# Kernel optimization log

Hardware: AMD Instinct MI355X
Metric: run time of the kernel (lower is better)

Reference implementation:

```python
import jax, jax.numpy as jnp
import numpy as np

B, D, A = 512, 32, 10
NUM_CODES, CODE_DIM = 512, 64
COMMIT = 0.25


def _conv(x, w, b):
    # NHWC input, HWIO kernel, SAME padding, stride 1 (flax nn.Conv defaults)
    y = jax.lax.conv_general_dilated(x, w, (1, 1), 'SAME',
                                     dimension_numbers=('NHWC', 'HWIO', 'NHWC'))
    return y + b


def setup_inputs() -> dict:
    key = jax.random.key(0)
    ks = jax.random.split(key, 16)
    def rn(k, shape, scale):
        return jax.random.normal(k, shape, dtype=jnp.float32) * scale
    inp = {
        'x': rn(ks[0], (B, D, D), 1.0),
        'conv1_w': rn(ks[1], (3, 3, 1, 32), 0.3),
        'conv1_b': jnp.zeros((32,), jnp.float32),
        'conv2_w': rn(ks[2], (3, 3, 32, 64), 0.06),
        'conv2_b': jnp.zeros((64,), jnp.float32),
        'codebook': rn(ks[3], (NUM_CODES, CODE_DIM), 0.12),  # variance_scaling fan_in-ish
        'w1': rn(ks[4], (D * D * 64, 128), 0.004),
        'b1': jnp.zeros((128,), jnp.float32),
        'w2': rn(ks[5], (128, 128), 0.09),
        'b2': jnp.zeros((128,), jnp.float32),
        'w3': rn(ks[6], (128, 128), 0.09),
        'b3': jnp.zeros((128,), jnp.float32),
        'wa1': rn(ks[7], (128, 128), 0.09),
        'ba1': jnp.zeros((128,), jnp.float32),
        'wa2': rn(ks[8], (128, A), 0.09),
        'ba2': jnp.zeros((A,), jnp.float32),
        'wc1': rn(ks[9], (128, 128), 0.09),
        'bc1': jnp.zeros((128,), jnp.float32),
        'wc2': rn(ks[10], (128, 128), 0.09),
        'bc2': jnp.zeros((128,), jnp.float32),
        'wc3': rn(ks[11], (128, 1), 0.09),
        'bc3': jnp.zeros((1,), jnp.float32),
    }
    return inp


def reference(x, conv1_w, conv1_b, conv2_w, conv2_b, codebook,
              w1, b1, w2, b2, w3, b3,
              wa1, ba1, wa2, ba2,
              wc1, bc1, wc2, bc2, wc3, bc3):
    h = x.reshape(-1, D, D, 1)
    h = jax.nn.relu(_conv(h, conv1_w, conv1_b))
    h = jax.nn.relu(_conv(h, conv2_w, conv2_b))  # [B, D, D, 64]

    # --- Vector quantization (cdist + argmin + gather, straight-through) ---
    flat = h.reshape(-1, CODE_DIM)  # [B*D*D, 64]
    distances = (jnp.sum(flat ** 2, axis=1, keepdims=True)
                 - 2.0 * flat @ codebook.T
                 + jnp.sum(codebook ** 2, axis=1)[None, :])  # [N, num_codes]
    encoding_indices = jnp.argmin(distances, axis=1)
    quantized = codebook[encoding_indices].reshape(h.shape)
    quantized = h + jax.lax.stop_gradient(quantized - h)  # straight-through
    e_latent = jnp.mean((jax.lax.stop_gradient(quantized) - h) ** 2)
    q_latent = jnp.mean((quantized - jax.lax.stop_gradient(h)) ** 2)
    vq_loss = q_latent + COMMIT * e_latent

    # --- MLP trunk + actor-critic heads ---
    emb = quantized.reshape(quantized.shape[0], -1)
    emb = jax.nn.relu(emb @ w1 + b1)
    emb = jax.nn.relu(emb @ w2 + b2)
    emb = jax.nn.relu(emb @ w3 + b3)

    a = jax.nn.relu(emb @ wa1 + ba1)
    probs = jax.nn.softmax(a @ wa2 + ba2, axis=-1)  # Categorical probs

    c = jax.nn.relu(emb @ wc1 + bc1)
    c = jax.nn.relu(c @ wc2 + bc2)
    value = jnp.squeeze(c @ wc3 + bc3, axis=-1)

    return probs, value, vq_loss, encoding_indices
```

## Files before the change

kernel.cpp:

```cpp
#include <hip/hip_runtime.h>
#include <math.h>

#define NB 512
#define DD 32
#define NPX 1024
#define NTOT 524288
#define NC 512
#define CD 64

typedef float v2f __attribute__((ext_vector_type(2)));
typedef _Float16 hf;
typedef hf hf8 __attribute__((ext_vector_type(8)));
typedef float f32x4 __attribute__((ext_vector_type(4)));

__device__ __forceinline__ v2f pkfma(v2f a, v2f b, v2f c) {
    return __builtin_elementwise_fma(a, b, c);
}
__device__ __forceinline__ v2f splat2(float s) { v2f r; r.x = s; r.y = s; return r; }

__device__ __forceinline__ f32x4 mfma16(hf8 a, hf8 b, f32x4 c) {
    return __builtin_amdgcn_mfma_f32_16x16x32_f16(a, b, c, 0, 0, 0);
}

__device__ __forceinline__ float np_sumsq64(const float* a, int stride) {
    float r[8];
    #pragma unroll
    for (int j = 0; j < 8; ++j) {
        float v = a[j * stride];
        r[j] = __fmul_rn(v, v);
    }
    #pragma unroll
    for (int i = 1; i < 8; ++i)
        #pragma unroll
        for (int j = 0; j < 8; ++j) {
            float v = a[(i * 8 + j) * stride];
            r[j] = __fadd_rn(r[j], __fmul_rn(v, v));
        }
    return __fadd_rn(__fadd_rn(__fadd_rn(r[0], r[1]), __fadd_rn(r[2], r[3])),
                     __fadd_rn(__fadd_rn(r[4], r[5]), __fadd_rn(r[6], r[7])));
}

__global__ __launch_bounds__(256) void k_conv1(const float* __restrict__ x,
                                               const float* __restrict__ w,
                                               const float* __restrict__ bias,
                                               float* __restrict__ h1,
                                               const float* __restrict__ cb,
                                               const float* __restrict__ c2w,
                                               const float* __restrict__ w1,
                                               float* __restrict__ cnorm,
                                               hf* __restrict__ cbh,
                                               hf* __restrict__ cbl,
                                               hf* __restrict__ wTh,
                                               hf* __restrict__ wTl,
                                               hf* __restrict__ w1h,
                                               hf* __restrict__ w1l,
                                               float* __restrict__ accv) {
    const int b = blockIdx.x;
    const int tid = threadIdx.x;
    {
        int t = b * 256 + tid;
        if (t < NC)
            cnorm[t] = np_sumsq64(cb + (size_t)t * CD, 1);
        if (b < 128) {
            float a = cb[t] * 256.f;
            hf h0 = (hf)a;
            float rl = (a - (float)h0) * 2048.f;
            cbh[t] = h0;
            cbl[t] = (hf)rl;
        }
        if (b >= 128 && b < 200) {
            int t2 = (b - 128) * 256 + tid;
            if (t2 < 18432) {
                int s9 = t2 >> 11, rem = t2 & 2047;
                int co = rem >> 5, ci = rem & 31;
                float a = c2w[s9 * 2048 + ci * 64 + co] * 256.f;
                hf h0 = (hf)a;
                float rl = (a - (float)h0) * 2048.f;
                wTh[t2] = h0;
                wTl[t2] = (hf)rl;
            }
        }
        if (b >= 200 && b < 456) {
            int t3 = (b - 200) * 256 + tid;
            int n = t3 & 127;
            int k8b = (t3 >> 7) * 16;
            for (int kk = 0; kk < 16; ++kk) {
                int k8 = k8b + kk;
                hf vh[8], vl[8];
                #pragma unroll
                for (int j = 0; j < 8; ++j) {
                    float a = w1[(size_t)(k8 * 8 + j) * 128 + n] * 256.f;
                    hf h0 = (hf)a;
                    float rl = (a - (float)h0) * 2048.f;
                    vh[j] = h0;
                    vl[j] = (hf)rl;
                }
                *(hf8*)(w1h + (size_t)k8 * 1024 + n * 8) = *(hf8*)vh;
                *(hf8*)(w1l + (size_t)k8 * 1024 + n * 8) = *(hf8*)vl;
            }
        }
        if (t == 0) accv[0] = 0.f;
    }
    __shared__ float xs[34][34];
    for (int i = tid; i < 34 * 34; i += 256) {
        int yy = i / 34, xx = i - yy * 34;
        float v = 0.f;
        if (yy >= 1 && yy <= 32 && xx >= 1 && xx <= 32)
            v = x[(size_t)b * NPX + (yy - 1) * 32 + (xx - 1)];
        xs[yy][xx] = v;
    }
    __syncthreads();
    for (int rep = 0; rep < 4; ++rep) {
        int px = tid + rep * 256;
        int y = px >> 5, xc = px & 31;
        v2f acc2[16];
        #pragma unroll
        for (int c = 0; c < 16; ++c) acc2[c] = splat2(0.f);
        #pragma unroll
        for (int dy = 0; dy < 3; ++dy)
        #pragma unroll
        for (int dx = 0; dx < 3; ++dx) {
            float a = xs[y + dy][xc + dx];
            v2f av = splat2(a);
            const v2f* wr = (const v2f*)(w + (dy * 3 + dx) * 32);
            #pragma unroll
            for (int c = 0; c < 16; ++c) acc2[c] = pkfma(av, wr[c], acc2[c]);
        }
        float4* out = (float4*)(h1 + ((size_t)b * NPX + px) * 32);
        #pragma unroll
        for (int q = 0; q < 8; ++q) {
            float4 v;
            v.x = fmaxf(__fadd_rn(acc2[q*2+0].x, bias[q*4+0]), 0.f);
            v.y = fmaxf(__fadd_rn(acc2[q*2+0].y, bias[q*4+1]), 0.f);
            v.z = fmaxf(__fadd_rn(acc2[q*2+1].x, bias[q*4+2]), 0.f);
            v.w = fmaxf(__fadd_rn(acc2[q*2+1].y, bias[q*4+3]), 0.f);
            out[q] = v;
        }
    }
}

#define CI_P 40
#define TAU 2e-4f
__global__ __launch_bounds__(512, 2) void k_cvq(const float* __restrict__ h1,
                                                const hf* __restrict__ wTh,
                                                const hf* __restrict__ wTl,
                                                const float* __restrict__ c2w,
                                                const float* __restrict__ c2b,
                                                const float* __restrict__ cb,
                                                const hf* __restrict__ cbh,
                                                const hf* __restrict__ cbl,
                                                const float* __restrict__ cnorm,
                                                int* __restrict__ idxout,
                                                float* __restrict__ fidx,
                                                float* __restrict__ lossacc) {
    __shared__ hf Ah[10 * 34 * CI_P];
    __shared__ hf Al[10 * 34 * CI_P];
    __shared__ float4 Ats[16][256];
    __shared__ float cn_lds[512];
    __shared__ int   mis_lds[256];
    __shared__ int   rlist[256];
    __shared__ float hex[8][64];
    __shared__ int   rcnt;
    const int blk = blockIdx.x;
    const int b = blk >> 2, strip = blk & 3;
    const int r0 = strip * 8;
    const int tid = threadIdx.x;
    const size_t base = (size_t)blk * 256;
    if (tid == 0) rcnt = 0;
    cn_lds[tid] = cnorm[tid];
    for (int i = tid; i < 640; i += 512) {
        int ci = i & 31, rem = i >> 5;
        int ry = rem >> 1, colx = (rem & 1) * 33;
        int idx = (ry * 34 + colx) * CI_P + ci;
        Ah[idx] = (hf)0.f;
        Al[idx] = (hf)0.f;
    }
    #pragma unroll
    for (int r = 0; r < 5; ++r) {
        int j = tid + r * 512;
        int ci4 = j & 7, xc = (j >> 3) & 31, ry = j >> 8;
        int gy = r0 - 1 + ry;
        float4 v = make_float4(0.f, 0.f, 0.f, 0.f);
        if (gy >= 0 && gy < 32)
            v = *(const float4*)(h1 + ((size_t)b * NPX + gy * 32 + xc) * 32 + ci4 * 4);
        int bi = (ry * 34 + xc + 1) * CI_P + ci4 * 4;
        float fv[4] = {v.x, v.y, v.z, v.w};
        #pragma unroll
        for (int q = 0; q < 4; ++q) {
            float a = fv[q] * 256.f;
            hf h0 = (hf)a;
            float rl = (a - (float)h0) * 2048.f;
            Ah[bi + q] = h0;
            Al[bi + q] = (hf)rl;
        }
    }
    __syncthreads();
    const int w = tid >> 6, l = tid & 63;
    const int co16 = l & 15, g = l >> 4;
    #pragma unroll 1
    for (int ntp = 0; ntp < 2; ++ntp) {
        f32x4 hi[2][2], mid[2][2], llt[2][2];
        #pragma unroll
        for (int s = 0; s < 2; ++s)
            #pragma unroll
            for (int n = 0; n < 2; ++n) {
                hi[s][n] = f32x4{0.f, 0.f, 0.f, 0.f};
                mid[s][n] = f32x4{0.f, 0.f, 0.f, 0.f};
                llt[s][n] = f32x4{0.f, 0.f, 0.f, 0.f};
            }
        #pragma unroll 1
        for (int s9 = 0; s9 < 9; ++s9) {
            const int dy = s9 / 3, dx = s9 - dy * 3;
            hf8 a_h[2], a_l[2];
            #pragma unroll
            for (int s = 0; s < 2; ++s) {
                int ofs = ((w + dy) * 34 + (s * 16 + co16 + dx)) * CI_P + 8 * g;
                a_h[s] = *(const hf8*)(Ah + ofs);
                a_l[s] = *(const hf8*)(Al + ofs);
            }
            #pragma unroll
            for (int ntl = 0; ntl < 2; ++ntl) {
                const int nt = ntp * 2 + ntl;
                const int wofs = (s9 * 64 + nt * 16 + co16) * 32 + 8 * g;
                const hf8 b_h = *(const hf8*)(wTh + wofs);
                const hf8 b_l = *(const hf8*)(wTl + wofs);
                #pragma unroll
                for (int s = 0; s < 2; ++s) {
                    hi[s][ntl]  = mfma16(a_h[s], b_h, hi[s][ntl]);
                    mid[s][ntl] = mfma16(a_h[s], b_l, mid[s][ntl]);
                    mid[s][ntl] = mfma16(a_l[s], b_h, mid[s][ntl]);
                    llt[s][ntl] = mfma16(a_l[s], b_l, llt[s][ntl]);
                }
            }
        }
        #pragma unroll
        for (int ntl = 0; ntl < 2; ++ntl) {
            const int co = (ntp * 2 + ntl) * 16 + co16;
            const float bco = c2b[co];
            #pragma unroll
            for (int s = 0; s < 2; ++s) {
                #pragma unroll
                for (int r = 0; r < 4; ++r) {
                    float comb = fmaf(mid[s][ntl][r], 4.8828125e-4f,
                                 fmaf(llt[s][ntl][r], 2.384185791015625e-7f,
                                      hi[s][ntl][r]));
                    float hv = fmaxf(
                        __fadd_rn(__fmul_rn(comb, 1.52587890625e-5f), bco), 0.f);
                    int pxl = w * 32 + s * 16 + g * 4 + r;
                    ((float*)&Ats[co >> 2][pxl])[co & 3] = hv;
                }
            }
        }
    }
    __syncthreads();
    const int co = co16;
    const int pxw = w * 32;
    hf8 ah[2][2], al[2][2];
    #pragma unroll
    for (int s = 0; s < 2; ++s)
        #pragma unroll
        for (int ks = 0; ks < 2; ++ks) {
            float4 q0 = Ats[ks * 8 + g * 2 + 0][pxw + s * 16 + co];
            float4 q1 = Ats[ks * 8 + g * 2 + 1][pxw + s * 16 + co];
            float fv[8] = {q0.x, q0.y, q0.z, q0.w, q1.x, q1.y, q1.z, q1.w};
            #pragma unroll
            for (int j = 0; j < 8; ++j) {
                float fa = fv[j] * 256.f;
                hf h0 = (hf)fa;
                float rl = (fa - (float)h0) * 2048.f;
                ah[s][ks][j] = h0;
                al[s][ks][j] = (hf)rl;
            }
        }
    float minv[2][4], min2[2][4];
    int   mini[2][4];
    #pragma unroll
    for (int s = 0; s < 2; ++s)
        #pragma unroll
        for (int r = 0; r < 4; ++r) {
            minv[s][r] = 3.4e38f; min2[s][r] = 3.4e38f; mini[s][r] = 0;
        }
    const hf* pbh = cbh + (size_t)co * 64 + g * 8;
    const hf* pbl = cbl + (size_t)co * 64 + g * 8;
    #pragma unroll 1
    for (int t = 0; t < 32; ++t) {
        const hf8 bh0 = *(const hf8*)(pbh + (size_t)t * 1024);
        const hf8 bh1 = *(const hf8*)(pbh + (size_t)t * 1024 + 32);
        const hf8 bl0 = *(const hf8*)(pbl + (size_t)t * 1024);
        const hf8 bl1 = *(const hf8*)(pbl + (size_t)t * 1024 + 32);
        const float cn = cn_lds[t * 16 + co];
        #pragma unroll
        for (int s = 0; s < 2; ++s) {
            f32x4 hi = {0.f, 0.f, 0.f, 0.f};
            f32x4 lo = {0.f, 0.f, 0.f, 0.f};
            f32x4 ll = {0.f, 0.f, 0.f, 0.f};
            lo = mfma16(ah[s][0], bl0, lo);
            lo = mfma16(al[s][0], bh0, lo);
            ll = mfma16(al[s][0], bl0, ll);
            hi = mfma16(ah[s][0], bh0, hi);
            lo = mfma16(ah[s][1], bl1, lo);
            lo = mfma16(al[s][1], bh1, lo);
            ll = mfma16(al[s][1], bl1, ll);
            hi = mfma16(ah[s][1], bh1, hi);
            #pragma unroll
            for (int r = 0; r < 4; ++r) {
                float comb = fmaf(lo[r], 4.8828125e-4f,
                             fmaf(ll[r], 2.384185791015625e-7f, hi[r]));
                float d = __fsub_rn(cn, __fmul_rn(3.0517578125e-5f, comb));
                if (d < minv[s][r]) {
                    min2[s][r] = minv[s][r];
                    minv[s][r] = d; mini[s][r] = t * 16 + co;
                } else if (d < min2[s][r]) {
                    min2[s][r] = d;
                }
            }
        }
    }
    #pragma unroll
    for (int s = 0; s < 2; ++s)
        #pragma unroll
        for (int r = 0; r < 4; ++r) {
            float v1 = minv[s][r], v2 = min2[s][r];
            int i1 = mini[s][r];
            #pragma unroll
            for (int off = 1; off < 16; off <<= 1) {
                float vo  = __shfl_xor(v1, off, 64);
                int   io  = __shfl_xor(i1, off, 64);
                float v2o = __shfl_xor(v2, off, 64);
                if (vo < v1 || (vo == v1 && io < i1)) {
                    v2 = fminf(v1, v2o);
                    v1 = vo; i1 = io;
                } else {
                    v2 = fminf(v2, vo);
                }
            }
            if (co == 0) {
                int pxo = pxw + s * 16 + g * 4 + r;
                mis_lds[pxo] = i1;
                if (v2 - v1 <= TAU) {
                    int slot = atomicAdd(&rcnt, 1);
                    rlist[slot] = pxo;
                }
            }
        }
    __syncthreads();
    const int nresc = rcnt;
    for (int rr = w; rr < nresc; rr += 8) {
        const int px = rlist[rr];
        const int gpx = (int)base + px;
        const int bimg = gpx >> 10, pp = gpx & 1023;
        const int py = pp >> 5, pxx = pp & 31;
        float* hx = &hex[w][0];
        {
            float acc = 0.f;
            #pragma unroll 1
            for (int s9 = 0; s9 < 9; ++s9) {
                const int dy = s9 / 3, dx = s9 - dy * 3;
                const int gy = py + dy - 1, gx = pxx + dx - 1;
                if (gy >= 0 && gy < 32 && gx >= 0 && gx < 32) {
                    const float* hp = h1 + ((size_t)bimg * NPX + gy * 32 + gx) * 32;
                    const float* wp = c2w + s9 * 2048 + l;
                    #pragma unroll
                    for (int ci = 0; ci < 32; ++ci)
                        acc = fmaf(hp[ci], wp[ci * 64], acc);
                }
            }
            hx[l] = fmaxf(__fadd_rn(acc, c2b[l]), 0.f);
        }
        const float Hp = np_sumsq64(hx, 1);
        float bv = 3.4e38f; int bi2 = 0;
        const float* crow = cb + (size_t)(l * 8) * 64;
        #pragma unroll 1
        for (int c = 0; c < 8; ++c) {
            float acc0 = 0.f;
            const float* cr = crow + c * 64;
            #pragma unroll
            for (int kg = 0; kg < 16; ++kg) {
                acc0 = fmaf(hx[kg*4+0], cr[kg*4+0], acc0);
                acc0 = fmaf(hx[kg*4+1], cr[kg*4+1], acc0);
                acc0 = fmaf(hx[kg*4+2], cr[kg*4+2], acc0);
                acc0 = fmaf(hx[kg*4+3], cr[kg*4+3], acc0);
            }
            float d = __fadd_rn(__fsub_rn(Hp, __fmul_rn(2.f, acc0)),
                                cn_lds[l * 8 + c]);
            if (d < bv) { bv = d; bi2 = l * 8 + c; }
        }
        #pragma unroll
        for (int off = 1; off < 64; off <<= 1) {
            float vo = __shfl_xor(bv, off, 64);
            int   io = __shfl_xor(bi2, off, 64);
            if (vo < bv || (vo == bv && io < bi2)) { bv = vo; bi2 = io; }
        }
        if (l == 0) mis_lds[px] = bi2;
    }
    __syncthreads();
    if (tid < 256) {
        int bi = mis_lds[tid];
        idxout[base + tid] = bi;
        fidx[base + tid] = (float)bi;
        float ls = 0.f;
        const float* crow = cb + (size_t)bi * 64;
        #pragma unroll
        for (int kg = 0; kg < 16; ++kg) {
            float4 a = Ats[kg][tid];
            float d0 = crow[kg*4+0] - a.x;
            float d1 = crow[kg*4+1] - a.y;
            float d2 = crow[kg*4+2] - a.z;
            float d3 = crow[kg*4+3] - a.w;
            ls = fmaf(d0, d0, ls); ls = fmaf(d1, d1, ls);
            ls = fmaf(d2, d2, ls); ls = fmaf(d3, d3, ls);
        }
        #pragma unroll
        for (int off = 32; off > 0; off >>= 1)
            ls += __shfl_down(ls, off, 64);
        if ((tid & 63) == 0) atomicAdd(lossacc, ls);
    }
}

__global__ __launch_bounds__(256) void k_fc1(const int* __restrict__ idxw,
                                             const hf* __restrict__ cbh,
                                             const hf* __restrict__ cbl,
                                             const hf* __restrict__ w1h,
                                             const hf* __restrict__ w1l,
                                             float* __restrict__ part) {
    const int kchunk = blockIdx.x;
    const int mtile  = blockIdx.y;
    const int tid = threadIdx.x;
    const int w = tid >> 6, l = tid & 63;
    const int co = l & 15, g = l >> 4;
    const int mbase = mtile * 64 + w * 16;
    f32x4 hi[8], mid[8];
    #pragma unroll
    for (int n = 0; n < 8; ++n) {
        hi[n] = f32x4{0.f, 0.f, 0.f, 0.f};
        mid[n] = f32x4{0.f, 0.f, 0.f, 0.f};
    }
    int code = 0;
    #pragma unroll 1
    for (int kstep = 0; kstep < 32; ++kstep) {
        if ((kstep & 1) == 0) {
            const int pix = kchunk * 16 + (kstep >> 1);
            code = idxw[(size_t)(mbase + co) * NPX + pix];
        }
        const int koff = (kstep & 1) * 32 + g * 8;
        const hf8 ah = *(const hf8*)(cbh + ((size_t)code << 6) + koff);
        const hf8 al = *(const hf8*)(cbl + ((size_t)code << 6) + koff);
        const size_t k8b = (size_t)(kchunk * 128 + kstep * 4 + g) * 1024;
        #pragma unroll
        for (int n = 0; n < 8; ++n) {
            const hf8 bh = *(const hf8*)(w1h + k8b + (n * 16 + co) * 8);
            const hf8 bl = *(const hf8*)(w1l + k8b + (n * 16 + co) * 8);
            hi[n]  = mfma16(ah, bh, hi[n]);
            mid[n] = mfma16(ah, bl, mid[n]);
            mid[n] = mfma16(al, bh, mid[n]);
        }
    }
    #pragma unroll
    for (int n = 0; n < 8; ++n)
        #pragma unroll
        for (int r = 0; r < 4; ++r) {
            float comb = fmaf(mid[n][r], 4.8828125e-4f, hi[n][r]);
            const int img = mtile * 64 + w * 16 + g * 4 + r;
            part[((size_t)kchunk * 512 + img) * 128 + n * 16 + co] =
                __fmul_rn(comb, 1.52587890625e-5f);
        }
}

__global__ __launch_bounds__(256) void k_reduce(const float* __restrict__ part,
                                                const float* __restrict__ b1,
                                                float* __restrict__ x0) {
    int t = blockIdx.x * 256 + threadIdx.x;
    float s = b1[t & 127];
    for (int ch = 0; ch < 64; ++ch)
        s += part[(size_t)ch * 65536 + t];
    x0[t] = fmaxf(s, 0.f);
}

__device__ __forceinline__ void mlp_layer(const float in[][16], float out[][16],
                                          const float* __restrict__ W,
                                          const float* __restrict__ bias,
                                          int tid, bool dorelu) {
    const int lane = tid & 63, wv = tid >> 6;
    const int img = lane & 15, cg = lane >> 4;
    const int c0 = wv * 32 + cg * 8;
    float acc[8] = {0,0,0,0,0,0,0,0};
    for (int k = 0; k < 128; ++k) {
        float a = in[k][img];
        float4 wA = *(const float4*)(W + (size_t)k * 128 + c0);
        float4 wB = *(const float4*)(W + (size_t)k * 128 + c0 + 4);
        acc[0] = fmaf(a, wA.x, acc[0]);
        acc[1] = fmaf(a, wA.y, acc[1]);
        acc[2] = fmaf(a, wA.z, acc[2]);
        acc[3] = fmaf(a, wA.w, acc[3]);
        acc[4] = fmaf(a, wB.x, acc[4]);
        acc[5] = fmaf(a, wB.y, acc[5]);
        acc[6] = fmaf(a, wB.z, acc[6]);
        acc[7] = fmaf(a, wB.w, acc[7]);
    }
    #pragma unroll
    for (int c = 0; c < 8; ++c) {
        float v = acc[c] + bias[c0 + c];
        if (dorelu) v = fmaxf(v, 0.f);
        out[c0 + c][img] = v;
    }
}

__global__ __launch_bounds__(256) void k_trunk(const float* __restrict__ x0,
        const float* __restrict__ w2, const float* __restrict__ b2,
        const float* __restrict__ w3, const float* __restrict__ b3,
        const float* __restrict__ wa1, const float* __restrict__ ba1,
        const float* __restrict__ wa2, const float* __restrict__ ba2,
        const float* __restrict__ wc1, const float* __restrict__ bc1,
        const float* __restrict__ wc2, const float* __restrict__ bc2,
        const float* __restrict__ wc3, const float* __restrict__ bc3,
        float* __restrict__ probs, float* __restrict__ value,
        const float* __restrict__ accv, float* __restrict__ vqloss) {
    __shared__ float bufA[128][16], bufB[128][16], bufC[128][16];
    __shared__ float lg[16][10];
    const int tid = threadIdx.x;
    const int m0 = blockIdx.x * 16;
    if (blockIdx.x == 0 && tid == 0)
        vqloss[0] = accv[0] * 1.25f / 33554432.f;
    for (int r = 0; r < 2; ++r) {
        int j = tid + r * 256;
        int img = j >> 5, k4 = j & 31;
        float4 v = *(const float4*)(x0 + (size_t)(m0 + img) * 128 + k4 * 4);
        bufA[k4*4+0][img] = v.x;
        bufA[k4*4+1][img] = v.y;
        bufA[k4*4+2][img] = v.z;
        bufA[k4*4+3][img] = v.w;
    }
    __syncthreads();
    mlp_layer(bufA, bufB, w2, b2, tid, true);   __syncthreads();
    mlp_layer(bufB, bufC, w3, b3, tid, true);   __syncthreads();
    mlp_layer(bufC, bufA, wa1, ba1, tid, true); __syncthreads();
    if (tid < 160) {
        int img = tid & 15, col = tid >> 4;
        float s = 0.f;
        for (int k = 0; k < 128; ++k)
            s = fmaf(bufA[k][img], wa2[(size_t)k * 10 + col], s);
        lg[img][col] = s + ba2[col];
    }
    __syncthreads();
    if (tid < 16) {
        int img = tid;
        float m = lg[img][0];
        #pragma unroll
        for (int c = 1; c < 10; ++c) m = fmaxf(m, lg[img][c]);
        float e[10]; float s = 0.f;
        #pragma unroll
        for (int c = 0; c < 10; ++c) { e[c] = expf(lg[img][c] - m); s += e[c]; }
        float inv = 1.f / s;
        #pragma unroll
        for (int c = 0; c < 10; ++c)
            probs[(size_t)(m0 + img) * 10 + c] = e[c] * inv;
    }
    __syncthreads();
    mlp_layer(bufC, bufB, wc1, bc1, tid, true); __syncthreads();
    mlp_layer(bufB, bufA, wc2, bc2, tid, true); __syncthreads();
    if (tid < 16) {
        int img = tid;
        float s = 0.f;
        for (int k = 0; k < 128; ++k)
            s = fmaf(bufA[k][img], wc3[k], s);
        value[m0 + img] = s + bc3[0];
    }
}

extern "C" void kernel_launch(void* const* d_in, const int* in_sizes, int n_in,
                              void* d_out, int out_size, void* d_ws, size_t ws_size,
                              hipStream_t stream) {
    const float* x   = (const float*)d_in[0];
    const float* c1w = (const float*)d_in[1];
    const float* c1b = (const float*)d_in[2];
    const float* c2w = (const float*)d_in[3];
    const float* c2b = (const float*)d_in[4];
    const float* cb  = (const float*)d_in[5];
    const float* w1  = (const float*)d_in[6];
    const float* b1  = (const float*)d_in[7];
    const float* w2  = (const float*)d_in[8];
    const float* b2  = (const float*)d_in[9];
    const float* w3  = (const float*)d_in[10];
    const float* b3  = (const float*)d_in[11];
    const float* wa1 = (const float*)d_in[12];
    const float* ba1 = (const float*)d_in[13];
    const float* wa2 = (const float*)d_in[14];
    const float* ba2 = (const float*)d_in[15];
    const float* wc1 = (const float*)d_in[16];
    const float* bc1 = (const float*)d_in[17];
    const float* wc2 = (const float*)d_in[18];
    const float* bc2 = (const float*)d_in[19];
    const float* wc3 = (const float*)d_in[20];
    const float* bc3 = (const float*)d_in[21];

    float* out = (float*)d_out;
    float* ws  = (float*)d_ws;

    float* h1    = ws;
    float* part  = ws;
    float* x0    = ws + (size_t)4 * 1024 * 1024;
    hf*    w1Th  = (hf*)(ws + (size_t)16777216);
    hf*    w1Tl  = (hf*)(ws + (size_t)20971520);
    int*   idxw  = (int*)(ws + (size_t)50331648);
    float* cn    = ws + (size_t)50855936;
    float* accv  = ws + (size_t)50856448;
    hf*    cbh   = (hf*)(ws + (size_t)50857984);
    hf*    cbl   = (hf*)(ws + (size_t)50874368);
    hf*    wTh   = (hf*)(ws + (size_t)50890752);
    hf*    wTl   = (hf*)(ws + (size_t)50899968);

    hipLaunchKernelGGL(k_conv1,  dim3(512),   dim3(256), 0, stream, x, c1w, c1b, h1,
                       cb, c2w, w1, cn, cbh, cbl, wTh, wTl, w1Th, w1Tl, accv);
    hipLaunchKernelGGL(k_cvq,    dim3(2048),  dim3(512), 0, stream, h1, wTh, wTl,
                       c2w, c2b, cb, cbh, cbl, cn, idxw, out + 5633, accv);
    hipLaunchKernelGGL(k_fc1,    dim3(64, 8), dim3(256), 0, stream, idxw, cbh, cbl,
                       w1Th, w1Tl, part);
    hipLaunchKernelGGL(k_reduce, dim3(256),   dim3(256), 0, stream, part, b1, x0);
    hipLaunchKernelGGL(k_trunk,  dim3(32),    dim3(256), 0, stream, x0,
                       w2, b2, w3, b3, wa1, ba1, wa2, ba2,
                       wc1, bc1, wc2, bc2, wc3, bc3,
                       out, out + 5120, accv, out + 5632);
}
```

Measured before the change: 710.5 us.

## Load conv2 input directly from global memory instead of staging halo tile in LDS

Removes the LDS staging of the fp16 hi/lo split conv2 input tile and its barrier. Each MFMA A-fragment is now read straight from global h1 and split into hi/lo in registers. Boundary pixels are handled by clamping addresses and zero-scaling. The lower LDS use lets launch bounds ask for 4 blocks per CU, trading redundant global/L2 reads and repeated conversions across the 9 taps and both n-tile passes for higher occupancy.

```diff
diff --git a/kernel.cpp b/kernel.cpp
--- a/kernel.cpp
+++ b/kernel.cpp
@@ -139,9 +139,8 @@
     }
 }
 
-#define CI_P 40
 #define TAU 2e-4f
-__global__ __launch_bounds__(512, 2) void k_cvq(const float* __restrict__ h1,
+__global__ __launch_bounds__(512, 4) void k_cvq(const float* __restrict__ h1,
                                                 const hf* __restrict__ wTh,
                                                 const hf* __restrict__ wTl,
                                                 const float* __restrict__ c2w,
@@ -153,8 +152,6 @@
                                                 int* __restrict__ idxout,
                                                 float* __restrict__ fidx,
                                                 float* __restrict__ lossacc) {
-    __shared__ hf Ah[10 * 34 * CI_P];
-    __shared__ hf Al[10 * 34 * CI_P];
     __shared__ float4 Ats[16][256];
     __shared__ float cn_lds[512];
     __shared__ int   mis_lds[256];
@@ -168,33 +165,6 @@
     const size_t base = (size_t)blk * 256;
     if (tid == 0) rcnt = 0;
     cn_lds[tid] = cnorm[tid];
-    for (int i = tid; i < 640; i += 512) {
-        int ci = i & 31, rem = i >> 5;
-        int ry = rem >> 1, colx = (rem & 1) * 33;
-        int idx = (ry * 34 + colx) * CI_P + ci;
-        Ah[idx] = (hf)0.f;
-        Al[idx] = (hf)0.f;
-    }
-    #pragma unroll
-    for (int r = 0; r < 5; ++r) {
-        int j = tid + r * 512;
-        int ci4 = j & 7, xc = (j >> 3) & 31, ry = j >> 8;
-        int gy = r0 - 1 + ry;
-        float4 v = make_float4(0.f, 0.f, 0.f, 0.f);
-        if (gy >= 0 && gy < 32)
-            v = *(const float4*)(h1 + ((size_t)b * NPX + gy * 32 + xc) * 32 + ci4 * 4);
-        int bi = (ry * 34 + xc + 1) * CI_P + ci4 * 4;
-        float fv[4] = {v.x, v.y, v.z, v.w};
-        #pragma unroll
-        for (int q = 0; q < 4; ++q) {
-            float a = fv[q] * 256.f;
-            hf h0 = (hf)a;
-            float rl = (a - (float)h0) * 2048.f;
-            Ah[bi + q] = h0;
-            Al[bi + q] = (hf)rl;
-        }
-    }
-    __syncthreads();
     const int w = tid >> 6, l = tid & 63;
     const int co16 = l & 15, g = l >> 4;
     #pragma unroll 1
@@ -211,12 +181,28 @@
         #pragma unroll 1
         for (int s9 = 0; s9 < 9; ++s9) {
             const int dy = s9 / 3, dx = s9 - dy * 3;
+            const int gy = r0 + w + dy - 1;
+            const bool rowok = (gy >= 0 && gy < 32);
+            const int gyc = rowok ? gy : 0;
             hf8 a_h[2], a_l[2];
             #pragma unroll
             for (int s = 0; s < 2; ++s) {
-                int ofs = ((w + dy) * 34 + (s * 16 + co16 + dx)) * CI_P + 8 * g;
-                a_h[s] = *(const hf8*)(Ah + ofs);
-                a_l[s] = *(const hf8*)(Al + ofs);
+                const int gx = s * 16 + co16 + dx - 1;
+                const bool ok = rowok && (gx >= 0) && (gx < 32);
+                const int gxc = (gx < 0) ? 0 : ((gx > 31) ? 31 : gx);
+                const float* hp = h1 + ((size_t)b * NPX + gyc * 32 + gxc) * 32 + 8 * g;
+                const float4 v0 = *(const float4*)(hp);
+                const float4 v1 = *(const float4*)(hp + 4);
+                const float vs = ok ? 256.f : 0.f;
+                float fv[8] = {v0.x, v0.y, v0.z, v0.w, v1.x, v1.y, v1.z, v1.w};
+                #pragma unroll
+                for (int j = 0; j < 8; ++j) {
+                    float fa = fv[j] * vs;
+                    hf h0 = (hf)fa;
+                    float rl = (fa - (float)h0) * 2048.f;
+                    a_h[s][j] = h0;
+                    a_l[s][j] = (hf)rl;
+                }
             }
             #pragma unroll
             for (int ntl = 0; ntl < 2; ++ntl) {
```

New measurement: 785.5 us. 1.11x slower.
